# Optimization experiments

Measured on AMD Instinct MI355X. Metric: run time of the kernel, lower is better.

## Reference

```python
import jax, jax.numpy as jnp
import numpy as np

IN, HID, BATCH = 1024, 1024, 4096


def _linear_params(key, out_dim, in_dim):
    # torch.nn.Linear default init: U(-1/sqrt(in), 1/sqrt(in))
    k1, k2 = jax.random.split(key)
    bound = 1.0 / np.sqrt(in_dim)
    w = jax.random.uniform(k1, (out_dim, in_dim), jnp.float32, -bound, bound)
    b = jax.random.uniform(k2, (out_dim,), jnp.float32, -bound, bound)
    return w, b


def setup_inputs() -> dict:
    key = jax.random.key(0)
    keys = jax.random.split(key, 11)
    inp = {
        'input': jax.random.normal(keys[0], (BATCH, IN), jnp.float32),
        'h': jax.random.normal(keys[1], (BATCH, HID), jnp.float32),
        'c': jax.random.normal(keys[2], (BATCH, HID), jnp.float32),
    }
    names = ['i_i', 'i_h', 'f_i', 'f_h', 'g_i', 'g_h', 'o_i', 'o_h']
    for n, k in zip(names, keys[3:]):
        in_dim = IN if n.endswith('_i') else HID
        w, b = _linear_params(k, HID, in_dim)
        inp['w_' + n] = w
        inp['b_' + n] = b
    return inp


def reference(input, h, c,
              w_i_i, b_i_i, w_i_h, b_i_h,
              w_f_i, b_f_i, w_f_h, b_f_h,
              w_g_i, b_g_i, w_g_h, b_g_h,
              w_o_i, b_o_i, w_o_h, b_o_h):
    def lin(x, w, b):
        return x @ w.T + b

    i = jax.nn.sigmoid(lin(input, w_i_i, b_i_i) + lin(h, w_i_h, b_i_h))
    f = jax.nn.sigmoid(lin(input, w_f_i, b_f_i) + lin(h, w_f_h, b_f_h))
    g = jnp.tanh(lin(input, w_g_i, b_g_i) + lin(h, w_g_h, b_g_h))
    o = jax.nn.sigmoid(lin(input, w_o_i, b_o_i) + lin(h, w_o_h, b_o_h))
    c_prime = f * c + i * g
    h_prime = o * jnp.tanh(c_prime)
    return (h_prime, c_prime)
```

## Files before the change

kernel.cpp:

```cpp
#include <hip/hip_runtime.h>
#include <stdint.h>

#define BATCH 4096
#define IN_DIM 1024
#define HID 1024
#define KDIM 2048
#define NGATE 4096

typedef __attribute__((ext_vector_type(4))) float floatx4;
typedef __attribute__((ext_vector_type(8))) __bf16 bf16x8;
typedef __attribute__((ext_vector_type(8))) unsigned short ushort8;

__device__ __forceinline__ unsigned short f2bf(float f) {
    union { float f; unsigned int u; } v; v.f = f;
    unsigned int u = v.u;
    u += 0x7fffu + ((u >> 16) & 1u);
    return (unsigned short)(u >> 16);
}
__device__ __forceinline__ float bf2f(unsigned short s) {
    union { unsigned int u; float f; } v; v.u = ((unsigned int)s) << 16;
    return v.f;
}
__device__ __forceinline__ ushort8 cvt8(const float* __restrict__ src) {
    float4 v0 = ((const float4*)src)[0];
    float4 v1 = ((const float4*)src)[1];
    ushort8 o = { f2bf(v0.x), f2bf(v0.y), f2bf(v0.z), f2bf(v0.w),
                  f2bf(v1.x), f2bf(v1.y), f2bf(v1.z), f2bf(v1.w) };
    return o;
}

__global__ __launch_bounds__(256) void prep_kernel(
    const float* __restrict__ x,  const float* __restrict__ h,
    const float* __restrict__ wii, const float* __restrict__ wih,
    const float* __restrict__ wfi, const float* __restrict__ wfh,
    const float* __restrict__ wgi, const float* __restrict__ wgh,
    const float* __restrict__ woi, const float* __restrict__ woh,
    const float* __restrict__ bii, const float* __restrict__ bih,
    const float* __restrict__ bfi, const float* __restrict__ bfh,
    const float* __restrict__ bgi, const float* __restrict__ bgh,
    const float* __restrict__ boi, const float* __restrict__ boh,
    unsigned short* __restrict__ Xb,
    unsigned short* __restrict__ Wb,
    float* __restrict__ bias)
{
    const int bid = blockIdx.x;
    const int tid = threadIdx.x;

    if (bid < 2048) {
        const int e = (bid * 256 + tid) * 8;
        const int b = e >> 10, k = e & 1023;
        *(ushort8*)(Xb + (size_t)b * KDIM + k) = cvt8(x + e);
    } else if (bid < 4096) {
        const int e = ((bid - 2048) * 256 + tid) * 8;
        const int b = e >> 10, k = e & 1023;
        *(ushort8*)(Xb + (size_t)b * KDIM + 1024 + k) = cvt8(h + e);
    } else if (bid < 8192) {
        const int m   = (bid - 4096) >> 9;
        const int off = (bid - 4096) & 511;
        const int e = (off * 256 + tid) * 8;
        const int n = e >> 10, k = e & 1023;
        const float* src;
        switch (m) {
            case 0: src = wii; break; case 1: src = wih; break;
            case 2: src = wfi; break; case 3: src = wfh; break;
            case 4: src = wgi; break; case 5: src = wgh; break;
            case 6: src = woi; break; default: src = woh; break;
        }
        const int gate = m >> 1, part = m & 1;
        *(ushort8*)(Wb + (size_t)(gate * 1024 + n) * KDIM + part * 1024 + k)
            = cvt8(src + e);
    } else {
        const int t = (bid - 8192) * 256 + tid;
        const int gate = (bid - 8192) >> 2;
        const int n = t & 1023;
        const float *bi, *bh_;
        switch (gate) {
            case 0: bi = bii; bh_ = bih; break;
            case 1: bi = bfi; bh_ = bfh; break;
            case 2: bi = bgi; bh_ = bgh; break;
            default: bi = boi; bh_ = boh; break;
        }
        bias[t] = bi[n] + bh_[n];
    }
}

#define GLD16(g, l)                                                          \
    __builtin_amdgcn_global_load_lds(                                        \
        (__attribute__((address_space(1))) void*)(g),                        \
        (__attribute__((address_space(3))) void*)(l), 16, 0, 0)

__global__ __launch_bounds__(256) void gemm_gates(
    const unsigned short* __restrict__ X,
    const unsigned short* __restrict__ W,
    const float* __restrict__ bias,
    unsigned short* __restrict__ G)
{
    __shared__ __align__(16) unsigned short As[128 * 32];
    __shared__ __align__(16) unsigned short Bs[128 * 32];

    const int tid  = threadIdx.x;
    const int wave = tid >> 6;
    const int lane = tid & 63;
    const int quad = lane >> 4, idx = lane & 15;
    const int wm = (wave >> 1) * 64, wn = (wave & 1) * 64;

    const int rowA0 = blockIdx.x * 128;
    const int rowB0 = blockIdx.y * 128;

    const int srow = tid >> 2, skk = (tid & 3) * 8;
    const unsigned short* gA0 = X + (size_t)(rowA0 + srow) * KDIM + skk;
    const unsigned short* gA1 = X + (size_t)(rowA0 + 64 + srow) * KDIM + skk;
    const unsigned short* gB0 = W + (size_t)(rowB0 + srow) * KDIM + skk;
    const unsigned short* gB1 = W + (size_t)(rowB0 + 64 + srow) * KDIM + skk;

    floatx4 acc[4][4] = {};

    for (int k0 = 0; k0 < KDIM; k0 += 32) {
        GLD16(gA0 + k0, As + tid * 8);
        GLD16(gA1 + k0, As + 2048 + tid * 8);
        GLD16(gB0 + k0, Bs + tid * 8);
        GLD16(gB1 + k0, Bs + 2048 + tid * 8);
        __syncthreads();

        bf16x8 af[4], bfr[4];
#pragma unroll
        for (int i = 0; i < 4; ++i)
            af[i] = *(const bf16x8*)(As + (wm + i * 16 + idx) * 32 + quad * 8);
#pragma unroll
        for (int j = 0; j < 4; ++j)
            bfr[j] = *(const bf16x8*)(Bs + (wn + j * 16 + idx) * 32 + quad * 8);
#pragma unroll
        for (int i = 0; i < 4; ++i)
#pragma unroll
            for (int j = 0; j < 4; ++j)
                acc[i][j] = __builtin_amdgcn_mfma_f32_16x16x32_bf16(
                    af[i], bfr[j], acc[i][j], 0, 0, 0);
        __syncthreads();
    }

#pragma unroll
    for (int j = 0; j < 4; ++j) {
        const int col = rowB0 + wn + j * 16 + idx;
        const float bv = bias[col];
        const int gate = col >> 10;
#pragma unroll
        for (int i = 0; i < 4; ++i) {
#pragma unroll
            for (int r = 0; r < 4; ++r) {
                const int row = rowA0 + wm + i * 16 + quad * 4 + r;
                const float v = acc[i][j][r] + bv;
                float a;
                if (gate == 2) {
                    const float e = __expf(2.f * v);
                    a = (e - 1.f) / (e + 1.f);
                } else {
                    a = 1.f / (1.f + __expf(-v));
                }
                G[(size_t)row * NGATE + col] = f2bf(a);
            }
        }
    }
}

__global__ __launch_bounds__(256) void ew_kernel(
    const unsigned short* __restrict__ G,
    const float* __restrict__ c,
    float* __restrict__ out)
{
    const int t = (blockIdx.x * 256 + threadIdx.x) * 8;
    const int b = t >> 10, n = t & 1023;
    const unsigned short* g = G + (size_t)b * NGATE;
    ushort8 iv8 = *(const ushort8*)(g + n);
    ushort8 fv8 = *(const ushort8*)(g + 1024 + n);
    ushort8 gv8 = *(const ushort8*)(g + 2048 + n);
    ushort8 ov8 = *(const ushort8*)(g + 3072 + n);
    float cp[8], hp[8];
#pragma unroll
    for (int e = 0; e < 8; ++e) {
        const float cv = c[t + e];
        const float cpe = bf2f(fv8[e]) * cv + bf2f(iv8[e]) * bf2f(gv8[e]);
        const float e2 = __expf(2.f * cpe);
        cp[e] = cpe;
        hp[e] = bf2f(ov8[e]) * ((e2 - 1.f) / (e2 + 1.f));
    }
    float* oh = out + t;
    float* oc = out + (size_t)BATCH * HID + t;
#pragma unroll
    for (int e = 0; e < 8; ++e) { oh[e] = hp[e]; oc[e] = cp[e]; }
}

extern "C" void kernel_launch(void* const* d_in, const int* in_sizes, int n_in,
                              void* d_out, int out_size, void* d_ws, size_t ws_size,
                              hipStream_t stream) {
    const float* x   = (const float*)d_in[0];
    const float* h   = (const float*)d_in[1];
    const float* c   = (const float*)d_in[2];
    const float* wii = (const float*)d_in[3];
    const float* bii = (const float*)d_in[4];
    const float* wih = (const float*)d_in[5];
    const float* bih = (const float*)d_in[6];
    const float* wfi = (const float*)d_in[7];
    const float* bfi = (const float*)d_in[8];
    const float* wfh = (const float*)d_in[9];
    const float* bfh = (const float*)d_in[10];
    const float* wgi = (const float*)d_in[11];
    const float* bgi = (const float*)d_in[12];
    const float* wgh = (const float*)d_in[13];
    const float* bgh = (const float*)d_in[14];
    const float* woi = (const float*)d_in[15];
    const float* boi = (const float*)d_in[16];
    const float* woh = (const float*)d_in[17];
    const float* boh = (const float*)d_in[18];

    char* ws = (char*)d_ws;
    unsigned short* Xb  = (unsigned short*)ws;
    unsigned short* Wb  = (unsigned short*)(ws + ((size_t)16 << 20));
    float*          bsv = (float*)(ws + ((size_t)32 << 20));
    unsigned short* G   = (unsigned short*)(ws + ((size_t)32 << 20) + 65536);

    prep_kernel<<<8208, 256, 0, stream>>>(
        x, h, wii, wih, wfi, wfh, wgi, wgh, woi, woh,
        bii, bih, bfi, bfh, bgi, bgh, boi, boh, Xb, Wb, bsv);

    dim3 g2(BATCH / 128, NGATE / 128);
    gemm_gates<<<g2, 256, 0, stream>>>(Xb, Wb, bsv, G);

    ew_kernel<<<BATCH * HID / (256 * 8), 256, 0, stream>>>(G, c, (float*)d_out);
}
```

Measured before the change: 255.9 us.

## Interleave gate weights and fuse LSTM elementwise into GEMM epilogue

Weight rows and biases are reordered so the four gates of each hidden unit sit next to each other in the GEMM output columns. Each GEMM tile can then compute c' and h' directly in its epilogue through an LDS staging buffer. This removes the bf16 gate matrix round-trip through global memory and the separate elementwise kernel launch. In exchange the epilogue gets longer, LDS use grows to the padded pitch, and there is an extra barrier.

After: 242.3 us. -5.3%, faster.

```diff
diff --git a/kernel.cpp b/kernel.cpp
--- a/kernel.cpp
+++ b/kernel.cpp
@@ -6,6 +6,7 @@
 #define HID 1024
 #define KDIM 2048
 #define NGATE 4096
+#define EPITCH 136
 
 typedef __attribute__((ext_vector_type(4))) float floatx4;
 typedef __attribute__((ext_vector_type(8))) __bf16 bf16x8;
@@ -67,7 +68,7 @@
             case 6: src = woi; break; default: src = woh; break;
         }
         const int gate = m >> 1, part = m & 1;
-        *(ushort8*)(Wb + (size_t)(gate * 1024 + n) * KDIM + part * 1024 + k)
+        *(ushort8*)(Wb + (size_t)(n * 4 + gate) * KDIM + part * 1024 + k)
             = cvt8(src + e);
     } else {
         const int t = (bid - 8192) * 256 + tid;
@@ -80,7 +81,7 @@
             case 2: bi = bgi; bh_ = bgh; break;
             default: bi = boi; bh_ = boh; break;
         }
-        bias[t] = bi[n] + bh_[n];
+        bias[n * 4 + gate] = bi[n] + bh_[n];
     }
 }
 
@@ -89,14 +90,17 @@
         (__attribute__((address_space(1))) void*)(g),                        \
         (__attribute__((address_space(3))) void*)(l), 16, 0, 0)
 
-__global__ __launch_bounds__(256) void gemm_gates(
+__global__ __launch_bounds__(256) void gemm_lstm(
     const unsigned short* __restrict__ X,
     const unsigned short* __restrict__ W,
     const float* __restrict__ bias,
-    unsigned short* __restrict__ G)
+    const float* __restrict__ c_in,
+    float* __restrict__ out)
 {
-    __shared__ __align__(16) unsigned short As[128 * 32];
-    __shared__ __align__(16) unsigned short Bs[128 * 32];
+    __shared__ __align__(16) unsigned char smem[128 * EPITCH * 2];
+    unsigned short* As = (unsigned short*)smem;
+    unsigned short* Bs = (unsigned short*)(smem + 8192);
+    unsigned short* E  = (unsigned short*)smem;
 
     const int tid  = threadIdx.x;
     const int wave = tid >> 6;
@@ -138,55 +142,61 @@
         __syncthreads();
     }
 
+    const int g = idx & 3;
 #pragma unroll
     for (int j = 0; j < 4; ++j) {
-        const int col = rowB0 + wn + j * 16 + idx;
-        const float bv = bias[col];
-        const int gate = col >> 10;
+        const int col = wn + j * 16 + idx;
+        const float bv = bias[rowB0 + col];
 #pragma unroll
         for (int i = 0; i < 4; ++i) {
 #pragma unroll
             for (int r = 0; r < 4; ++r) {
-                const int row = rowA0 + wm + i * 16 + quad * 4 + r;
-                const float v = acc[i][j][r] + bv;
-                float a;
-                if (gate == 2) {
-                    const float e = __expf(2.f * v);
-                    a = (e - 1.f) / (e + 1.f);
-                } else {
-                    a = 1.f / (1.f + __expf(-v));
-                }
-                G[(size_t)row * NGATE + col] = f2bf(a);
+                const int row = wm + i * 16 + quad * 4 + r;
+                const float v  = acc[i][j][r] + bv;
+                const float vv = (g == 2) ? 2.f * v : v;
+                const float s  = 1.f / (1.f + __expf(-vv));
+                const float a  = (g == 2) ? 2.f * s - 1.f : s;
+                E[row * EPITCH + col] = f2bf(a);
             }
         }
     }
-}
-
-__global__ __launch_bounds__(256) void ew_kernel(
-    const unsigned short* __restrict__ G,
-    const float* __restrict__ c,
-    float* __restrict__ out)
-{
-    const int t = (blockIdx.x * 256 + threadIdx.x) * 8;
-    const int b = t >> 10, n = t & 1023;
-    const unsigned short* g = G + (size_t)b * NGATE;
-    ushort8 iv8 = *(const ushort8*)(g + n);
-    ushort8 fv8 = *(const ushort8*)(g + 1024 + n);
-    ushort8 gv8 = *(const ushort8*)(g + 2048 + n);
-    ushort8 ov8 = *(const ushort8*)(g + 3072 + n);
-    float cp[8], hp[8];
-#pragma unroll
-    for (int e = 0; e < 8; ++e) {
-        const float cv = c[t + e];
-        const float cpe = bf2f(fv8[e]) * cv + bf2f(iv8[e]) * bf2f(gv8[e]);
-        const float e2 = __expf(2.f * cpe);
-        cp[e] = cpe;
-        hp[e] = bf2f(ov8[e]) * ((e2 - 1.f) / (e2 + 1.f));
-    }
-    float* oh = out + t;
-    float* oc = out + (size_t)BATCH * HID + t;
-#pragma unroll
-    for (int e = 0; e < 8; ++e) { oh[e] = hp[e]; oc[e] = cp[e]; }
+    __syncthreads();
+
+    const int tid8 = tid & 7;
+    const int rowo = tid >> 3;
+    float* __restrict__ out_h = out;
+    float* __restrict__ out_c = out + (size_t)BATCH * HID;
+
+#pragma unroll
+    for (int p = 0; p < 4; ++p) {
+        const int row_l = p * 32 + rowo;
+        const int row_g = rowA0 + row_l;
+        const int colc  = tid8 * 16;
+        ushort8 e0 = *(const ushort8*)(E + row_l * EPITCH + colc);
+        ushort8 e1 = *(const ushort8*)(E + row_l * EPITCH + colc + 8);
+        const int u0 = (rowB0 >> 2) + tid8 * 4;
+        const float4 cv = *(const float4*)(c_in + (size_t)row_g * HID + u0);
+
+        float cvv[4] = { cv.x, cv.y, cv.z, cv.w };
+        float hp[4], cp[4];
+#pragma unroll
+        for (int d = 0; d < 4; ++d) {
+            const ushort8& e = (d < 2) ? e0 : e1;
+            const int b = (d & 1) * 4;
+            const float iv = bf2f(e[b + 0]);
+            const float fv = bf2f(e[b + 1]);
+            const float gv = bf2f(e[b + 2]);
+            const float ov = bf2f(e[b + 3]);
+            const float c2 = fv * cvv[d] + iv * gv;
+            const float e2 = __expf(2.f * c2);
+            cp[d] = c2;
+            hp[d] = ov * ((e2 - 1.f) / (e2 + 1.f));
+        }
+        float4 hv = { hp[0], hp[1], hp[2], hp[3] };
+        float4 cpv = { cp[0], cp[1], cp[2], cp[3] };
+        *(float4*)(out_h + (size_t)row_g * HID + u0) = hv;
+        *(float4*)(out_c + (size_t)row_g * HID + u0) = cpv;
+    }
 }
 
 extern "C" void kernel_launch(void* const* d_in, const int* in_sizes, int n_in,
@@ -216,14 +226,11 @@
     unsigned short* Xb  = (unsigned short*)ws;
     unsigned short* Wb  = (unsigned short*)(ws + ((size_t)16 << 20));
     float*          bsv = (float*)(ws + ((size_t)32 << 20));
-    unsigned short* G   = (unsigned short*)(ws + ((size_t)32 << 20) + 65536);
 
     prep_kernel<<<8208, 256, 0, stream>>>(
         x, h, wii, wih, wfi, wfh, wgi, wgh, woi, woh,
         bii, bih, bfi, bfh, bgi, bgh, boi, boh, Xb, Wb, bsv);
 
     dim3 g2(BATCH / 128, NGATE / 128);
-    gemm_gates<<<g2, 256, 0, stream>>>(Xb, Wb, bsv, G);
-
-    ew_kernel<<<BATCH * HID / (256 * 8), 256, 0, stream>>>(G, c, (float*)d_out);
-}
+    gemm_lstm<<<g2, 256, 0, stream>>>(Xb, Wb, bsv, c, (float*)d_out);
+}
```
